# Performance work log

Hardware: AMD Instinct MI355X
Metric: run time of the kernel (lower is better)

Reference implementation:

```python
import jax, jax.numpy as jnp
import numpy as np

D = 768
M = 10000
B, S = 4, 2048
SCALE = 1.0 / np.sqrt(D)
LN_EPS = 1e-5


def setup_inputs() -> dict:
    key = jax.random.key(0)
    ks = jax.random.split(key, 8)
    return {
        "current_states": jax.random.normal(ks[0], (B, S, D), jnp.float32),
        "memory": jax.random.normal(ks[1], (M, D), jnp.float32),
        "gate_w": jax.random.normal(ks[2], (2 * D, 1), jnp.float32) * 0.02,
        "gate_b": jnp.zeros((1,), jnp.float32),
        "fusion_w1": jax.random.normal(ks[3], (3 * D, D), jnp.float32) * 0.02,
        "fusion_b1": jnp.zeros((D,), jnp.float32),
        "fusion_w2": jax.random.normal(ks[4], (D, D), jnp.float32) * 0.02,
        "fusion_b2": jnp.zeros((D,), jnp.float32),
        "ln_gamma": jnp.ones((D,), jnp.float32),
        "ln_beta": jnp.zeros((D,), jnp.float32),
    }


def reference(current_states, memory, gate_w, gate_b,
              fusion_w1, fusion_b1, fusion_w2, fusion_b2,
              ln_gamma, ln_beta):
    # --- MemoryBank.read: content-addressable attention over fixed memory ---
    # similarity: [B, S, M]
    sim = jnp.einsum("bsd,md->bsm", current_states, memory) * SCALE
    attn = jax.nn.softmax(sim, axis=-1)
    retrieved = jnp.einsum("bsm,md->bsd", attn, memory)  # [B, S, D]

    # --- long-term gate + residual fusion ---
    gate_in = jnp.concatenate([current_states, retrieved], axis=-1)  # [B,S,2D]
    lt_gate = jax.nn.sigmoid(gate_in @ gate_w + gate_b)  # [B,S,1]
    x = current_states + lt_gate * retrieved

    # --- memory_fusion MLP (working memory absent on first step) ---
    combined = jnp.concatenate([x, x, retrieved], axis=-1)  # [B,S,3D]
    h = jax.nn.gelu(combined @ fusion_w1 + fusion_b1, approximate=False)
    h = h @ fusion_w2 + fusion_b2

    # LayerNorm over last dim
    mu = jnp.mean(h, axis=-1, keepdims=True)
    var = jnp.var(h, axis=-1, keepdims=True)
    out = (h - mu) * jax.lax.rsqrt(var + LN_EPS) * ln_gamma + ln_beta
    return out
```

## Files before the change

### kernel.cpp

```cpp
#include <hip/hip_runtime.h>
#include <math.h>

#define N_TOK 8192
#define DIM   768
#define MEMN  10000
#define MEMP  10240
#define TQ    64
#define TM    256
#define NSPLIT 2
#define TILES_PER_SPLIT 20

constexpr float SCALE = 0.036084391824351615f;

typedef short bf16x8 __attribute__((ext_vector_type(8)));
typedef float f32x4  __attribute__((ext_vector_type(4)));

__device__ __forceinline__ unsigned short f2bf(float f) {
    unsigned u = __float_as_uint(f);
    unsigned r = (u + 0x7fffu + ((u >> 16) & 1u)) >> 16;
    return (unsigned short)r;
}

__global__ __launch_bounds__(256)
void prep_all(const float* __restrict__ mem, const float* __restrict__ w1,
              const float* __restrict__ w2,
              unsigned short* __restrict__ memF, unsigned short* __restrict__ memS,
              unsigned short* __restrict__ w12T, unsigned short* __restrict__ w2T)
{
    __shared__ float T[32][65];
    const int bid = blockIdx.x;

    if (bid < 640) {
        const int mb = bid;
        const bool zero = (mb >= MEMN / 16);
#pragma unroll
        for (int it = 0; it < 6; ++it) {
            const int s   = it * 256 + threadIdx.x;
            const int kc  = s >> 6;
            const int r   = s & 63;
            const int l16 = r >> 2, q = r & 3;
            unsigned short o[8];
            if (!zero) {
                const float* src = &mem[(size_t)(mb * 16 + l16) * DIM + kc * 32 + q * 8];
                float4 v0 = *(const float4*)src;
                float4 v1 = *(const float4*)(src + 4);
                o[0] = f2bf(v0.x); o[1] = f2bf(v0.y); o[2] = f2bf(v0.z); o[3] = f2bf(v0.w);
                o[4] = f2bf(v1.x); o[5] = f2bf(v1.y); o[6] = f2bf(v1.z); o[7] = f2bf(v1.w);
            } else {
#pragma unroll
                for (int j = 0; j < 8; ++j) o[j] = 0;
            }
            *(uint4*)&memF[((size_t)mb * 24 + kc) * 512 + r * 8] = *(const uint4*)o;
        }
    } else if (bid < 4480) {
        const int rr = bid - 640;
        const int mc = rr % 320;
        const int d0 = (rr / 320) * 64;
        const int tx = threadIdx.x & 63;
        const int ty = threadIdx.x >> 6;
#pragma unroll
        for (int i = 0; i < 8; ++i) {
            const int row = ty + 4 * i;
            const int m   = mc * 32 + row;
            T[row][tx] = (m < MEMN) ? mem[(size_t)m * DIM + d0 + tx] : 0.f;
        }
        __syncthreads();
        const int dbl = threadIdx.x >> 6;
        const int r   = threadIdx.x & 63;
        const int l16 = r >> 2, q = r & 3;
        unsigned short o[8];
#pragma unroll
        for (int j = 0; j < 8; ++j) o[j] = f2bf(T[q * 8 + j][dbl * 16 + l16]);
        *(uint4*)&memS[((size_t)(d0 / 16 + dbl) * 320 + mc) * 512 + r * 8] = *(const uint4*)o;
    } else if (bid < 5632) {
        const int rr = bid - 4480;
        const int kb = (rr % 48) * 32;
        const int nb = (rr / 48) * 32;
        const int tx = threadIdx.x & 31, ty = threadIdx.x >> 5;
#pragma unroll
        for (int i = 0; i < 4; ++i) {
            int k = kb + ty + 8 * i;
            float v = w1[(size_t)(768 + k) * DIM + nb + tx];
            if (kb < 768) v += w1[(size_t)k * DIM + nb + tx];
            T[ty + 8 * i][tx] = v;
        }
        __syncthreads();
        if (threadIdx.x < 128) {
            const int sub = threadIdx.x >> 6;
            const int r   = threadIdx.x & 63;
            const int l16 = r >> 2, q = r & 3;
            unsigned short o[8];
#pragma unroll
            for (int j = 0; j < 8; ++j) o[j] = f2bf(T[q * 8 + j][sub * 16 + l16]);
            const int n16 = (nb >> 4) + sub;
            const int kc  = kb >> 5;
            *(uint4*)&w12T[((size_t)n16 * 48 + kc) * 512 + r * 8] = *(const uint4*)o;
        }
    } else {
        const int rr = bid - 5632;
        const int kb = (rr % 24) * 32;
        const int nb = (rr / 24) * 32;
        const int tx = threadIdx.x & 31, ty = threadIdx.x >> 5;
#pragma unroll
        for (int i = 0; i < 4; ++i)
            T[ty + 8 * i][tx] = w2[(size_t)(kb + ty + 8 * i) * DIM + nb + tx];
        __syncthreads();
        if (threadIdx.x < 128) {
            const int sub = threadIdx.x >> 6;
            const int r   = threadIdx.x & 63;
            const int l16 = r >> 2, q = r & 3;
            unsigned short o[8];
#pragma unroll
            for (int j = 0; j < 8; ++j) o[j] = f2bf(T[q * 8 + j][sub * 16 + l16]);
            const int n16 = (nb >> 4) + sub;
            const int kc  = kb >> 5;
            *(uint4*)&w2T[((size_t)n16 * 24 + kc) * 512 + r * 8] = *(const uint4*)o;
        }
    }
}

template <int PLAIN>
__global__ __launch_bounds__(1024, 4)
void attn_mfma(const float* __restrict__ cs, const unsigned short* __restrict__ memF,
               const unsigned short* __restrict__ memS,
               float* __restrict__ retrRaw, float* __restrict__ Lvec)
{
    __shared__ __align__(16) unsigned short Qs[64 * 768];
    __shared__ __align__(16) unsigned short Ps[64 * 256];
    __shared__ float Lred[16][64];

    const int tid    = threadIdx.x;
    const int w      = tid >> 6;
    const int lane   = tid & 63;
    const int quad   = lane >> 4;
    const int l16    = lane & 15;
    const int fr     = ((l16 << 2) | quad) << 3;

    const int split = blockIdx.y;
    const int q0    = blockIdx.x * TQ;

    const int dbase  = w * 48;
    const int mstrip = w * 16;

    {
        const int qr  = tid >> 4;
        const int db0 = tid & 15;
        const float* src = cs + (size_t)(q0 + qr) * DIM;
        const int sw = qr & 7;
#pragma unroll
        for (int i = 0; i < 6; ++i) {
            int db = db0 + i * 16;
            float4 v0 = *(const float4*)&src[db * 8];
            float4 v1 = *(const float4*)&src[db * 8 + 4];
            unsigned short o[8];
            o[0] = f2bf(v0.x); o[1] = f2bf(v0.y); o[2] = f2bf(v0.z); o[3] = f2bf(v0.w);
            o[4] = f2bf(v1.x); o[5] = f2bf(v1.y); o[6] = f2bf(v1.z); o[7] = f2bf(v1.w);
            *(uint4*)&Qs[qr * 768 + ((db ^ sw) << 3)] = *(const uint4*)o;
        }
    }
    __syncthreads();

    f32x4 oacc[4][3];
#pragma unroll
    for (int a = 0; a < 4; ++a)
#pragma unroll
        for (int b = 0; b < 3; ++b) oacc[a][b] = (f32x4){0.f, 0.f, 0.f, 0.f};
    float lsum[4][4];
#pragma unroll
    for (int a = 0; a < 4; ++a)
#pragma unroll
        for (int r = 0; r < 4; ++r) lsum[a][r] = 0.f;

    const int xsw = l16 & 7;

    for (int st = 0; st < TILES_PER_SPLIT; ++st) {
        const int m0  = (split * TILES_PER_SPLIT + st) * TM;
        const int mc0 = m0 >> 5;

        f32x4 sacc[4];
#pragma unroll
        for (int a = 0; a < 4; ++a) sacc[a] = (f32x4){0.f, 0.f, 0.f, 0.f};

        const unsigned short* fb = memF + ((size_t)(m0 >> 4) + w) * 12288 + fr;

        bf16x8 pb[2];
        pb[0] = *(const bf16x8*)(fb);
        pb[1] = *(const bf16x8*)(fb + 512);

#pragma unroll
        for (int ks = 0; ks < 24; ++ks) {
            const int xq = (((ks << 2) + quad) ^ xsw) << 3;
            bf16x8 a0 = *(const bf16x8*)&Qs[l16 * 768 + xq];
            bf16x8 a1 = *(const bf16x8*)&Qs[(16 + l16) * 768 + xq];
            bf16x8 a2 = *(const bf16x8*)&Qs[(32 + l16) * 768 + xq];
            bf16x8 a3 = *(const bf16x8*)&Qs[(48 + l16) * 768 + xq];
            bf16x8 b = pb[ks & 1];
            sacc[0] = __builtin_amdgcn_mfma_f32_16x16x32_bf16(a0, b, sacc[0], 0, 0, 0);
            sacc[1] = __builtin_amdgcn_mfma_f32_16x16x32_bf16(a1, b, sacc[1], 0, 0, 0);
            sacc[2] = __builtin_amdgcn_mfma_f32_16x16x32_bf16(a2, b, sacc[2], 0, 0, 0);
            sacc[3] = __builtin_amdgcn_mfma_f32_16x16x32_bf16(a3, b, sacc[3], 0, 0, 0);
            if (ks < 22) pb[ks & 1] = *(const bf16x8*)(fb + (ks + 2) * 512);
        }

        __syncthreads();

        {
            const int mloc = mstrip + l16;
            const bool ok  = (m0 + mloc) < MEMN;
#pragma unroll
            for (int qt = 0; qt < 4; ++qt)
#pragma unroll
                for (int r = 0; r < 4; ++r) {
                    float p = ok ? __expf(sacc[qt][r] * SCALE) : 0.f;
                    const int q = qt * 16 + quad * 4 + r;
                    lsum[qt][r] += p;
                    Ps[q * 256 + (((mloc >> 3) ^ (q & 7)) << 3) + (mloc & 7)] = f2bf(p);
                }
        }

        __syncthreads();

        const unsigned short* msp = memS + ((size_t)(3 * w) * 320 + mc0) * 512 + fr;
        bf16x8 cb[2][3];
#pragma unroll
        for (int nt = 0; nt < 3; ++nt) {
            cb[0][nt] = *(const bf16x8*)(msp + (size_t)nt * 163840);
            cb[1][nt] = *(const bf16x8*)(msp + (size_t)nt * 163840 + 512);
        }

#pragma unroll
        for (int ks = 0; ks < 8; ++ks) {
            const int xp = (((ks << 2) + quad) ^ xsw) << 3;
            bf16x8 pa0 = *(const bf16x8*)&Ps[l16 * 256 + xp];
            bf16x8 pa1 = *(const bf16x8*)&Ps[(16 + l16) * 256 + xp];
            bf16x8 pa2 = *(const bf16x8*)&Ps[(32 + l16) * 256 + xp];
            bf16x8 pa3 = *(const bf16x8*)&Ps[(48 + l16) * 256 + xp];
            const bool dopf = (ks < 6);
#pragma unroll
            for (int nt = 0; nt < 3; ++nt) {
                oacc[0][nt] = __builtin_amdgcn_mfma_f32_16x16x32_bf16(pa0, cb[ks & 1][nt], oacc[0][nt], 0, 0, 0);
                oacc[1][nt] = __builtin_amdgcn_mfma_f32_16x16x32_bf16(pa1, cb[ks & 1][nt], oacc[1][nt], 0, 0, 0);
                oacc[2][nt] = __builtin_amdgcn_mfma_f32_16x16x32_bf16(pa2, cb[ks & 1][nt], oacc[2][nt], 0, 0, 0);
                oacc[3][nt] = __builtin_amdgcn_mfma_f32_16x16x32_bf16(pa3, cb[ks & 1][nt], oacc[3][nt], 0, 0, 0);
                if (dopf) cb[ks & 1][nt] = *(const bf16x8*)(msp + (size_t)nt * 163840 + (ks + 2) * 512);
            }
        }
    }

    float* ob = retrRaw + (PLAIN ? (size_t)split * ((size_t)N_TOK * DIM) : (size_t)0);
#pragma unroll
    for (int qt = 0; qt < 4; ++qt)
#pragma unroll
        for (int nt = 0; nt < 3; ++nt)
#pragma unroll
            for (int r = 0; r < 4; ++r) {
                const size_t idx = (size_t)(q0 + qt * 16 + quad * 4 + r) * DIM + dbase + nt * 16 + l16;
                if (PLAIN)
                    ob[idx] = oacc[qt][nt][r];
                else
                    __hip_atomic_fetch_add(&ob[idx], oacc[qt][nt][r],
                                           __ATOMIC_RELAXED, __HIP_MEMORY_SCOPE_AGENT);
            }

#pragma unroll
    for (int qt = 0; qt < 4; ++qt)
#pragma unroll
        for (int r = 0; r < 4; ++r) {
            float v = lsum[qt][r];
#pragma unroll
            for (int off = 1; off < 16; off <<= 1) v += __shfl_xor(v, off);
            if (l16 == 0) {
                if (PLAIN)
                    Lred[w][qt * 16 + quad * 4 + r] = v;
                else
                    __hip_atomic_fetch_add(&Lvec[q0 + qt * 16 + quad * 4 + r], v,
                                           __ATOMIC_RELAXED, __HIP_MEMORY_SCOPE_AGENT);
            }
        }
    if (PLAIN) {
        __syncthreads();
        if (tid < 64) {
            float s = 0.f;
#pragma unroll
            for (int ww = 0; ww < 16; ++ww) s += Lred[ww][tid];
            Lvec[(size_t)split * N_TOK + q0 + tid] = s;
        }
    }
}

template <int PLAIN>
__global__ __launch_bounds__(512, 2)
void fused_tail(const float* __restrict__ retrRaw, const float* __restrict__ Lvec,
                const float* __restrict__ cs, const float* __restrict__ gw,
                const float* __restrict__ gb,
                const unsigned short* __restrict__ W12T, const float* __restrict__ fb1,
                const unsigned short* __restrict__ W2T,  const float* __restrict__ fb2,
                const float* __restrict__ gamma, const float* __restrict__ beta,
                float* __restrict__ out)
{
    __shared__ __align__(16) unsigned short XRl[6 * 4096];
    __shared__ __align__(16) unsigned short Hl[3 * 4096];
    __shared__ float red[2][8][16];

    const int tid  = threadIdx.x;
    const int w    = tid >> 6;
    const int lane = tid & 63;
    const int quad = lane >> 4;
    const int l16  = lane & 15;
    const int row0 = blockIdx.x * 16;
    const int nbase = w * 96;
    const int xsw3 = l16 & 7;
    const int fr   = ((l16 << 2) | quad) << 3;
    const int nb16 = w * 6;

#pragma unroll
    for (int it = 0; it < 2; ++it) {
        const int rl = it * 8 + w;
        const int row = row0 + rl;
        const float lv = PLAIN ? (Lvec[row] + Lvec[N_TOK + row]) : Lvec[row];
        const float rli = 1.0f / lv;
        const float* rr  = retrRaw + (size_t)row * DIM;
        const float* rr1 = retrRaw + (size_t)N_TOK * DIM + (size_t)row * DIM;
        const float* cr  = cs + (size_t)row * DIM;

        float4 rv[3], cv[3];
        float d = 0.f;
#pragma unroll
        for (int i = 0; i < 3; ++i) {
            const int c4 = i * 256 + lane * 4;
            float4 r = *(const float4*)&rr[c4];
            if (PLAIN) {
                float4 r1 = *(const float4*)&rr1[c4];
                r.x += r1.x; r.y += r1.y; r.z += r1.z; r.w += r1.w;
            }
            r.x *= rli; r.y *= rli; r.z *= rli; r.w *= rli;
            float4 c = *(const float4*)&cr[c4];
            float4 g1 = *(const float4*)&gw[c4];
            float4 g2 = *(const float4*)&gw[DIM + c4];
            d += c.x * g1.x + c.y * g1.y + c.z * g1.z + c.w * g1.w;
            d += r.x * g2.x + r.y * g2.y + r.z * g2.z + r.w * g2.w;
            rv[i] = r; cv[i] = c;
        }
#pragma unroll
        for (int off = 32; off > 0; off >>= 1) d += __shfl_xor(d, off);
        d += gb[0];
        const float g = 1.0f / (1.0f + __expf(-d));

        const int g8 = lane >> 1;
        const int lo = (lane & 1) * 4;
#pragma unroll
        for (int i = 0; i < 3; ++i) {
            ushort4 xo, ro;
            xo.x = f2bf(cv[i].x + g * rv[i].x); xo.y = f2bf(cv[i].y + g * rv[i].y);
            xo.z = f2bf(cv[i].z + g * rv[i].z); xo.w = f2bf(cv[i].w + g * rv[i].w);
            ro.x = f2bf(rv[i].x); ro.y = f2bf(rv[i].y);
            ro.z = f2bf(rv[i].z); ro.w = f2bf(rv[i].w);
            const int sw = ((g8 ^ (rl & 7)) << 3) + lo;
            *(ushort4*)&XRl[i * 4096 + rl * 256 + sw] = xo;
            *(ushort4*)&XRl[(3 + i) * 4096 + rl * 256 + sw] = ro;
        }
    }
    __syncthreads();

    f32x4 acc[6];
#pragma unroll
    for (int nt = 0; nt < 6; ++nt) acc[nt] = (f32x4){0.f, 0.f, 0.f, 0.f};

    bf16x8 b[6];
#pragma unroll
    for (int nt = 0; nt < 6; ++nt)
        b[nt] = *(const bf16x8*)&W12T[(size_t)(nb16 + nt) * 48 * 512 + fr];

#pragma unroll
    for (int ch = 0; ch < 6; ++ch) {
#pragma unroll
        for (int ks = 0; ks < 8; ++ks) {
            bf16x8 af = *(const bf16x8*)&XRl[ch * 4096 + l16 * 256 + ((((ks << 2) + quad) ^ xsw3) << 3)];
            int kn = ch * 8 + ks + 1;
            if (kn >= 48) kn = 0;
#pragma unroll
            for (int nt = 0; nt < 6; ++nt) {
                acc[nt] = __builtin_amdgcn_mfma_f32_16x16x32_bf16(af, b[nt], acc[nt], 0, 0, 0);
                b[nt] = *(const bf16x8*)&W12T[((size_t)(nb16 + nt) * 48 + kn) * 512 + fr];
            }
        }
    }

    {
        float bv[6];
#pragma unroll
        for (int nt = 0; nt < 6; ++nt) bv[nt] = fb1[nbase + nt * 16 + l16];
#pragma unroll
        for (int nt = 0; nt < 6; ++nt) {
            const int col = nbase + nt * 16 + l16;
            const int cch = col >> 8;
            const int g8  = (col >> 3) & 31;
#pragma unroll
            for (int r = 0; r < 4; ++r) {
                const int rowl = quad * 4 + r;
                float v = acc[nt][r] + bv[nt];
                v = 0.5f * v * (1.0f + erff(v * 0.7071067811865476f));
                Hl[cch * 4096 + rowl * 256 + ((g8 ^ (rowl & 7)) << 3) + (l16 & 7)] = f2bf(v);
            }
        }
    }

    bf16x8 b2[6];
#pragma unroll
    for (int nt = 0; nt < 6; ++nt)
        b2[nt] = *(const bf16x8*)&W2T[(size_t)(nb16 + nt) * 24 * 512 + fr];

    __syncthreads();

    f32x4 acc2[6];
#pragma unroll
    for (int nt = 0; nt < 6; ++nt) acc2[nt] = (f32x4){0.f, 0.f, 0.f, 0.f};

#pragma unroll
    for (int ch = 0; ch < 3; ++ch) {
#pragma unroll
        for (int ks = 0; ks < 8; ++ks) {
            bf16x8 af = *(const bf16x8*)&Hl[ch * 4096 + l16 * 256 + ((((ks << 2) + quad) ^ xsw3) << 3)];
            int kn = ch * 8 + ks + 1;
            if (kn >= 24) kn = 0;
#pragma unroll
            for (int nt = 0; nt < 6; ++nt) {
                acc2[nt] = __builtin_amdgcn_mfma_f32_16x16x32_bf16(af, b2[nt], acc2[nt], 0, 0, 0);
                b2[nt] = *(const bf16x8*)&W2T[((size_t)(nb16 + nt) * 24 + kn) * 512 + fr];
            }
        }
    }

    {
        float bv[6];
#pragma unroll
        for (int nt = 0; nt < 6; ++nt) bv[nt] = fb2[nbase + nt * 16 + l16];

        float v[6][4];
        float s1[4] = {0.f, 0.f, 0.f, 0.f}, s2[4] = {0.f, 0.f, 0.f, 0.f};
#pragma unroll
        for (int nt = 0; nt < 6; ++nt)
#pragma unroll
            for (int r = 0; r < 4; ++r) {
                float t = acc2[nt][r] + bv[nt];
                v[nt][r] = t;
                s1[r] += t;
                s2[r] += t * t;
            }
#pragma unroll
        for (int r = 0; r < 4; ++r) {
#pragma unroll
            for (int off = 1; off < 16; off <<= 1) {
                s1[r] += __shfl_xor(s1[r], off);
                s2[r] += __shfl_xor(s2[r], off);
            }
            if (l16 == 0) {
                red[0][w][quad * 4 + r] = s1[r];
                red[1][w][quad * 4 + r] = s2[r];
            }
        }
        __syncthreads();
#pragma unroll
        for (int r = 0; r < 4; ++r) {
            const int rl16 = quad * 4 + r;
            float t1 = 0.f, t2 = 0.f;
#pragma unroll
            for (int ww = 0; ww < 8; ++ww) {
                t1 += red[0][ww][rl16];
                t2 += red[1][ww][rl16];
            }
            const float mu  = t1 * (1.0f / 768.0f);
            const float var = fmaxf(t2 * (1.0f / 768.0f) - mu * mu, 0.f);
            const float rs  = rsqrtf(var + 1e-5f);
            const int row = row0 + rl16;
#pragma unroll
            for (int nt = 0; nt < 6; ++nt) {
                const int col = nbase + nt * 16 + l16;
                out[(size_t)row * DIM + col] = (v[nt][r] - mu) * rs * gamma[col] + beta[col];
            }
        }
    }
}

extern "C" void kernel_launch(void* const* d_in, const int* in_sizes, int n_in,
                              void* d_out, int out_size, void* d_ws, size_t ws_size,
                              hipStream_t stream)
{
    const float* cs  = (const float*)d_in[0];
    const float* mem = (const float*)d_in[1];
    const float* gw  = (const float*)d_in[2];
    const float* gb  = (const float*)d_in[3];
    const float* fw1 = (const float*)d_in[4];
    const float* fb1 = (const float*)d_in[5];
    const float* fw2 = (const float*)d_in[6];
    const float* fb2 = (const float*)d_in[7];
    const float* gam = (const float*)d_in[8];
    const float* bet = (const float*)d_in[9];
    float* out = (float*)d_out;

    char* ws = (char*)d_ws;
    const size_t PLAIN_WS = 97976320;
    const bool plain = (ws_size >= PLAIN_WS);

    unsigned short* memF = (unsigned short*)ws;
    unsigned short* memS = (unsigned short*)(ws + 15728640);
    float*          retr = (float*)(ws + 44040192);
    float*          Lvec;
    unsigned short* w12T;
    unsigned short* w2T;
    if (plain) {
        Lvec = (float*)(ws + 94371840);
        w12T = (unsigned short*)(ws + 94437376);
        w2T  = (unsigned short*)(ws + 96796672);
    } else {
        Lvec = (float*)(ws + 69206016);
        w12T = (unsigned short*)(ws + 69238784);
        w2T  = (unsigned short*)(ws + 71598080);
    }

    if (!plain)
        hipMemsetAsync(retr, 0, 25165824 + 32768, stream);

    prep_all<<<6208, 256, 0, stream>>>(mem, fw1, fw2, memF, memS, w12T, w2T);

    if (plain) {
        attn_mfma<1><<<dim3(N_TOK / TQ, NSPLIT), 1024, 0, stream>>>(cs, memF, memS, retr, Lvec);
        fused_tail<1><<<N_TOK / 16, 512, 0, stream>>>(retr, Lvec, cs, gw, gb,
                                                      w12T, fb1, w2T, fb2, gam, bet, out);
    } else {
        attn_mfma<0><<<dim3(N_TOK / TQ, NSPLIT), 1024, 0, stream>>>(cs, memF, memS, retr, Lvec);
        fused_tail<0><<<N_TOK / 16, 512, 0, stream>>>(retr, Lvec, cs, gw, gb,
                                                      w12T, fb1, w2T, fb2, gam, bet, out);
    }
}
```

Before: 826.0 us.

## Widen fused_tail block to 32 rows with 16 waves sharing weight fragments

After: 804.9 us. -2.6%, faster.

```diff
diff --git a/kernel.cpp b/kernel.cpp
--- a/kernel.cpp
+++ b/kernel.cpp
@@ -289,7 +289,7 @@
 }
 
 template <int PLAIN>
-__global__ __launch_bounds__(512, 2)
+__global__ __launch_bounds__(1024, 4)
 void fused_tail(const float* __restrict__ retrRaw, const float* __restrict__ Lvec,
                 const float* __restrict__ cs, const float* __restrict__ gw,
                 const float* __restrict__ gb,
@@ -298,24 +298,24 @@
                 const float* __restrict__ gamma, const float* __restrict__ beta,
                 float* __restrict__ out)
 {
-    __shared__ __align__(16) unsigned short XRl[6 * 4096];
-    __shared__ __align__(16) unsigned short Hl[3 * 4096];
-    __shared__ float red[2][8][16];
+    __shared__ __align__(16) unsigned short XRl[6 * 8192];
+    __shared__ __align__(16) unsigned short Hl[3 * 8192];
+    __shared__ float red[2][16][32];
 
     const int tid  = threadIdx.x;
     const int w    = tid >> 6;
     const int lane = tid & 63;
     const int quad = lane >> 4;
     const int l16  = lane & 15;
-    const int row0 = blockIdx.x * 16;
-    const int nbase = w * 96;
+    const int row0 = blockIdx.x * 32;
+    const int nbase = w * 48;
     const int xsw3 = l16 & 7;
     const int fr   = ((l16 << 2) | quad) << 3;
-    const int nb16 = w * 6;
+    const int nb16 = w * 3;
 
 #pragma unroll
     for (int it = 0; it < 2; ++it) {
-        const int rl = it * 8 + w;
+        const int rl = it * 16 + w;
         const int row = row0 + rl;
         const float lv = PLAIN ? (Lvec[row] + Lvec[N_TOK + row]) : Lvec[row];
         const float rli = 1.0f / lv;
@@ -356,129 +356,151 @@
             ro.x = f2bf(rv[i].x); ro.y = f2bf(rv[i].y);
             ro.z = f2bf(rv[i].z); ro.w = f2bf(rv[i].w);
             const int sw = ((g8 ^ (rl & 7)) << 3) + lo;
-            *(ushort4*)&XRl[i * 4096 + rl * 256 + sw] = xo;
-            *(ushort4*)&XRl[(3 + i) * 4096 + rl * 256 + sw] = ro;
+            *(ushort4*)&XRl[i * 8192 + rl * 256 + sw] = xo;
+            *(ushort4*)&XRl[(3 + i) * 8192 + rl * 256 + sw] = ro;
         }
     }
     __syncthreads();
 
-    f32x4 acc[6];
-#pragma unroll
-    for (int nt = 0; nt < 6; ++nt) acc[nt] = (f32x4){0.f, 0.f, 0.f, 0.f};
-
-    bf16x8 b[6];
-#pragma unroll
-    for (int nt = 0; nt < 6; ++nt)
+    f32x4 acc[2][3];
+#pragma unroll
+    for (int rt = 0; rt < 2; ++rt)
+#pragma unroll
+        for (int nt = 0; nt < 3; ++nt) acc[rt][nt] = (f32x4){0.f, 0.f, 0.f, 0.f};
+
+    bf16x8 b[3];
+#pragma unroll
+    for (int nt = 0; nt < 3; ++nt)
         b[nt] = *(const bf16x8*)&W12T[(size_t)(nb16 + nt) * 48 * 512 + fr];
 
 #pragma unroll
     for (int ch = 0; ch < 6; ++ch) {
 #pragma unroll
         for (int ks = 0; ks < 8; ++ks) {
-            bf16x8 af = *(const bf16x8*)&XRl[ch * 4096 + l16 * 256 + ((((ks << 2) + quad) ^ xsw3) << 3)];
+            const int xg = ((((ks << 2) + quad) ^ xsw3) << 3);
+            bf16x8 af0 = *(const bf16x8*)&XRl[ch * 8192 + l16 * 256 + xg];
+            bf16x8 af1 = *(const bf16x8*)&XRl[ch * 8192 + (16 + l16) * 256 + xg];
             int kn = ch * 8 + ks + 1;
             if (kn >= 48) kn = 0;
 #pragma unroll
-            for (int nt = 0; nt < 6; ++nt) {
-                acc[nt] = __builtin_amdgcn_mfma_f32_16x16x32_bf16(af, b[nt], acc[nt], 0, 0, 0);
+            for (int nt = 0; nt < 3; ++nt) {
+                acc[0][nt] = __builtin_amdgcn_mfma_f32_16x16x32_bf16(af0, b[nt], acc[0][nt], 0, 0, 0);
+                acc[1][nt] = __builtin_amdgcn_mfma_f32_16x16x32_bf16(af1, b[nt], acc[1][nt], 0, 0, 0);
                 b[nt] = *(const bf16x8*)&W12T[((size_t)(nb16 + nt) * 48 + kn) * 512 + fr];
             }
         }
     }
 
     {
-        float bv[6];
-#pragma unroll
-        for (int nt = 0; nt < 6; ++nt) bv[nt] = fb1[nbase + nt * 16 + l16];
-#pragma unroll
-        for (int nt = 0; nt < 6; ++nt) {
+        float bv[3];
+#pragma unroll
+        for (int nt = 0; nt < 3; ++nt) bv[nt] = fb1[nbase + nt * 16 + l16];
+#pragma unroll
+        for (int nt = 0; nt < 3; ++nt) {
             const int col = nbase + nt * 16 + l16;
             const int cch = col >> 8;
             const int g8  = (col >> 3) & 31;
 #pragma unroll
-            for (int r = 0; r < 4; ++r) {
-                const int rowl = quad * 4 + r;
-                float v = acc[nt][r] + bv[nt];
-                v = 0.5f * v * (1.0f + erff(v * 0.7071067811865476f));
-                Hl[cch * 4096 + rowl * 256 + ((g8 ^ (rowl & 7)) << 3) + (l16 & 7)] = f2bf(v);
-            }
-        }
-    }
-
-    bf16x8 b2[6];
-#pragma unroll
-    for (int nt = 0; nt < 6; ++nt)
+            for (int rt = 0; rt < 2; ++rt)
+#pragma unroll
+                for (int r = 0; r < 4; ++r) {
+                    const int rowl = rt * 16 + quad * 4 + r;
+                    float v = acc[rt][nt][r] + bv[nt];
+                    v = 0.5f * v * (1.0f + erff(v * 0.7071067811865476f));
+                    Hl[cch * 8192 + rowl * 256 + ((g8 ^ (rowl & 7)) << 3) + (l16 & 7)] = f2bf(v);
+                }
+        }
+    }
+
+    bf16x8 b2[3];
+#pragma unroll
+    for (int nt = 0; nt < 3; ++nt)
         b2[nt] = *(const bf16x8*)&W2T[(size_t)(nb16 + nt) * 24 * 512 + fr];
 
     __syncthreads();
 
-    f32x4 acc2[6];
-#pragma unroll
-    for (int nt = 0; nt < 6; ++nt) acc2[nt] = (f32x4){0.f, 0.f, 0.f, 0.f};
+    f32x4 acc2[2][3];
+#pragma unroll
+    for (int rt = 0; rt < 2; ++rt)
+#pragma unroll
+        for (int nt = 0; nt < 3; ++nt) acc2[rt][nt] = (f32x4){0.f, 0.f, 0.f, 0.f};
 
 #pragma unroll
     for (int ch = 0; ch < 3; ++ch) {
 #pragma unroll
         for (int ks = 0; ks < 8; ++ks) {
-            bf16x8 af = *(const bf16x8*)&Hl[ch * 4096 + l16 * 256 + ((((ks << 2) + quad) ^ xsw3) << 3)];
+            const int xg = ((((ks << 2) + quad) ^ xsw3) << 3);
+            bf16x8 af0 = *(const bf16x8*)&Hl[ch * 8192 + l16 * 256 + xg];
+            bf16x8 af1 = *(const bf16x8*)&Hl[ch * 8192 + (16 + l16) * 256 + xg];
             int kn = ch * 8 + ks + 1;
             if (kn >= 24) kn = 0;
 #pragma unroll
-            for (int nt = 0; nt < 6; ++nt) {
-                acc2[nt] = __builtin_amdgcn_mfma_f32_16x16x32_bf16(af, b2[nt], acc2[nt], 0, 0, 0);
+            for (int nt = 0; nt < 3; ++nt) {
+                acc2[0][nt] = __builtin_amdgcn_mfma_f32_16x16x32_bf16(af0, b2[nt], acc2[0][nt], 0, 0, 0);
+                acc2[1][nt] = __builtin_amdgcn_mfma_f32_16x16x32_bf16(af1, b2[nt], acc2[1][nt], 0, 0, 0);
                 b2[nt] = *(const bf16x8*)&W2T[((size_t)(nb16 + nt) * 24 + kn) * 512 + fr];
             }
         }
     }
 
     {
-        float bv[6];
-#pragma unroll
-        for (int nt = 0; nt < 6; ++nt) bv[nt] = fb2[nbase + nt * 16 + l16];
-
-        float v[6][4];
-        float s1[4] = {0.f, 0.f, 0.f, 0.f}, s2[4] = {0.f, 0.f, 0.f, 0.f};
-#pragma unroll
-        for (int nt = 0; nt < 6; ++nt)
+        float bv[3];
+#pragma unroll
+        for (int nt = 0; nt < 3; ++nt) bv[nt] = fb2[nbase + nt * 16 + l16];
+
+        float v[2][3][4];
+        float s1[2][4], s2[2][4];
+#pragma unroll
+        for (int rt = 0; rt < 2; ++rt)
+#pragma unroll
+            for (int r = 0; r < 4; ++r) { s1[rt][r] = 0.f; s2[rt][r] = 0.f; }
+#pragma unroll
+        for (int rt = 0; rt < 2; ++rt)
+#pragma unroll
+            for (int nt = 0; nt < 3; ++nt)
+#pragma unroll
+                for (int r = 0; r < 4; ++r) {
+                    float t = acc2[rt][nt][r] + bv[nt];
+                    v[rt][nt][r] = t;
+                    s1[rt][r] += t;
+                    s2[rt][r] += t * t;
+                }
+#pragma unroll
+        for (int rt = 0; rt < 2; ++rt)
 #pragma unroll
             for (int r = 0; r < 4; ++r) {
-                float t = acc2[nt][r] + bv[nt];
-                v[nt][r] = t;
-                s1[r] += t;
-                s2[r] += t * t;
-            }
-#pragma unroll
-        for (int r = 0; r < 4; ++r) {
-#pragma unroll
-            for (int off = 1; off < 16; off <<= 1) {
-                s1[r] += __shfl_xor(s1[r], off);
-                s2[r] += __shfl_xor(s2[r], off);
-            }
-            if (l16 == 0) {
-                red[0][w][quad * 4 + r] = s1[r];
-                red[1][w][quad * 4 + r] = s2[r];
-            }
-        }
-        __syncthreads();
-#pragma unroll
-        for (int r = 0; r < 4; ++r) {
-            const int rl16 = quad * 4 + r;
-            float t1 = 0.f, t2 = 0.f;
-#pragma unroll
-            for (int ww = 0; ww < 8; ++ww) {
-                t1 += red[0][ww][rl16];
-                t2 += red[1][ww][rl16];
-            }
-            const float mu  = t1 * (1.0f / 768.0f);
-            const float var = fmaxf(t2 * (1.0f / 768.0f) - mu * mu, 0.f);
-            const float rs  = rsqrtf(var + 1e-5f);
-            const int row = row0 + rl16;
-#pragma unroll
-            for (int nt = 0; nt < 6; ++nt) {
-                const int col = nbase + nt * 16 + l16;
-                out[(size_t)row * DIM + col] = (v[nt][r] - mu) * rs * gamma[col] + beta[col];
-            }
-        }
+#pragma unroll
+                for (int off = 1; off < 16; off <<= 1) {
+                    s1[rt][r] += __shfl_xor(s1[rt][r], off);
+                    s2[rt][r] += __shfl_xor(s2[rt][r], off);
+                }
+                if (l16 == 0) {
+                    red[0][w][rt * 16 + quad * 4 + r] = s1[rt][r];
+                    red[1][w][rt * 16 + quad * 4 + r] = s2[rt][r];
+                }
+            }
+        __syncthreads();
+#pragma unroll
+        for (int rt = 0; rt < 2; ++rt)
+#pragma unroll
+            for (int r = 0; r < 4; ++r) {
+                const int rl = rt * 16 + quad * 4 + r;
+                float t1 = 0.f, t2 = 0.f;
+#pragma unroll
+                for (int ww = 0; ww < 16; ++ww) {
+                    t1 += red[0][ww][rl];
+                    t2 += red[1][ww][rl];
+                }
+                const float mu  = t1 * (1.0f / 768.0f);
+                const float var = fmaxf(t2 * (1.0f / 768.0f) - mu * mu, 0.f);
+                const float rs  = rsqrtf(var + 1e-5f);
+                const int row = row0 + rl;
+#pragma unroll
+                for (int nt = 0; nt < 3; ++nt) {
+                    const int col = nbase + nt * 16 + l16;
+                    out[(size_t)row * DIM + col] = (v[rt][nt][r] - mu) * rs * gamma[col] + beta[col];
+                }
+            }
     }
 }
 
@@ -525,11 +547,11 @@
 
     if (plain) {
         attn_mfma<1><<<dim3(N_TOK / TQ, NSPLIT), 1024, 0, stream>>>(cs, memF, memS, retr, Lvec);
-        fused_tail<1><<<N_TOK / 16, 512, 0, stream>>>(retr, Lvec, cs, gw, gb,
-                                                      w12T, fb1, w2T, fb2, gam, bet, out);
+        fused_tail<1><<<N_TOK / 32, 1024, 0, stream>>>(retr, Lvec, cs, gw, gb,
+                                                       w12T, fb1, w2T, fb2, gam, bet, out);
     } else {
         attn_mfma<0><<<dim3(N_TOK / TQ, NSPLIT), 1024, 0, stream>>>(cs, memF, memS, retr, Lvec);
-        fused_tail<0><<<N_TOK / 16, 512, 0, stream>>>(retr, Lvec, cs, gw, gb,
-                                                      w12T, fb1, w2T, fb2, gam, bet, out);
+        fused_tail<0><<<N_TOK / 32, 1024, 0, stream>>>(retr, Lvec, cs, gw, gb,
+                                                       w12T, fb1, w2T, fb2, gam, bet, out);
     }
 }
```
